# Kernel optimization log

Hardware: AMD Instinct MI355X
Metric: run time of the kernel (lower is better)

The kernel has to match this reference:

```python
import jax, jax.numpy as jnp
import numpy as np

NUM_HEADS = 12
HEAD_DIM = 64
HIDDEN = NUM_HEADS * HEAD_DIM  # 768
B, L = 4, 512

def setup_inputs() -> dict:
    key = jax.random.key(0)
    ks = jax.random.split(key, 8)
    s = 0.02
    return {
        "hidden_states": jax.random.normal(ks[0], (B, L, HIDDEN), jnp.float32),
        "relation_embedding_k": jax.random.normal(ks[1], (B, L, L, HEAD_DIM), jnp.float32),
        "relation_embedding_v": jax.random.normal(ks[2], (B, L, L, HEAD_DIM), jnp.float32),
        "Wq": jax.random.normal(ks[3], (HIDDEN, HIDDEN), jnp.float32) * s,
        "bq": jnp.zeros((HIDDEN,), jnp.float32),
        "Wk": jax.random.normal(ks[4], (HIDDEN, HIDDEN), jnp.float32) * s,
        "bk": jnp.zeros((HIDDEN,), jnp.float32),
        "Wv": jax.random.normal(ks[5], (HIDDEN, HIDDEN), jnp.float32) * s,
        "bv": jnp.zeros((HIDDEN,), jnp.float32),
    }

def _heads(x):
    # [B, L, HIDDEN] -> [B, H, L, D]
    b, l, _ = x.shape
    return x.reshape(b, l, NUM_HEADS, HEAD_DIM).transpose(0, 2, 1, 3)

def reference(hidden_states, relation_embedding_k, relation_embedding_v,
              Wq, bq, Wk, bk, Wv, bv):
    q = _heads(hidden_states @ Wq + bq)  # [B,H,L,D]
    k = _heads(hidden_states @ Wk + bk)
    v = _heads(hidden_states @ Wv + bv)

    # content scores + relation key scores (shared across heads)
    scores = jnp.einsum('bhld,bhmd->bhlm', q, k)
    scores = scores + jnp.einsum('bhld,blrd->bhlr', q, relation_embedding_k)
    scores = scores / np.sqrt(HEAD_DIM).astype(np.float32)

    probs = jax.nn.softmax(scores, axis=-1)  # [B,H,L,L]

    ctx = jnp.einsum('bhlm,bhmd->bhld', probs, v)
    ctx = ctx + jnp.einsum('bhlr,brld->bhld', probs, relation_embedding_v)

    # [B,H,L,D] -> [B,L,HIDDEN]
    b, h, l, d = ctx.shape
    return ctx.transpose(0, 2, 1, 3).reshape(b, l, h * d)
```

## Files before the change

### kernel.cpp

```cpp
#include <hip/hip_runtime.h>
#include <stdint.h>


typedef __attribute__((ext_vector_type(8))) short bf16x8;
typedef __attribute__((ext_vector_type(4))) float f32x4;
typedef __attribute__((ext_vector_type(4))) unsigned int u32x4;

__device__ __forceinline__ unsigned short f2bf(float f) {
  union { float f; unsigned int u; } v; v.f = f;
  unsigned int r = v.u + 0x7fffu + ((v.u >> 16) & 1u);
  return (unsigned short)(r >> 16);
}
__device__ __forceinline__ float bf2f(unsigned short s) {
  union { unsigned int u; float f; } v; v.u = ((unsigned int)s) << 16;
  return v.f;
}
__device__ __forceinline__ void gload_lds16(const void* g, void* l) {
  __builtin_amdgcn_global_load_lds((const __attribute__((address_space(1))) void*)g,
                                   (__attribute__((address_space(3))) void*)l, 16, 0, 0);
}

__global__ void k_cvt_hidden(const float* __restrict__ x, unsigned short* __restrict__ y) {
  int i = blockIdx.x * 256 + threadIdx.x;
  float4 v = reinterpret_cast<const float4*>(x)[i];
  ushort4 o;
  o.x = f2bf(v.x); o.y = f2bf(v.y); o.z = f2bf(v.z); o.w = f2bf(v.w);
  reinterpret_cast<ushort4*>(y)[i] = o;
}

__global__ void k_transp_w(const float* __restrict__ Wq, const float* __restrict__ Wk,
                           const float* __restrict__ Wv, unsigned short* __restrict__ wt) {
  __shared__ float t[64][65];
  const int kt = blockIdx.x, nt = blockIdx.y, wsel = blockIdx.z;
  const float* W = wsel == 0 ? Wq : (wsel == 1 ? Wk : Wv);
  const int lx = threadIdx.x & 63, ly = threadIdx.x >> 6;
  for (int i = 0; i < 64; i += 4)
    t[ly + i][lx] = W[(size_t)(kt * 64 + ly + i) * 768 + nt * 64 + lx];
  __syncthreads();
  for (int i = 0; i < 64; i += 4) {
    int r = ly + i;
    wt[((size_t)wsel * 768 + nt * 64 + r) * 768 + kt * 64 + lx] = f2bf(t[lx][r]);
  }
}

__global__ __launch_bounds__(256) void k_qkv_gemm(
    const unsigned short* __restrict__ A,
    const unsigned short* __restrict__ Bt,
    const float* __restrict__ bq, const float* __restrict__ bk, const float* __restrict__ bv,
    unsigned short* __restrict__ qbf,
    unsigned short* __restrict__ kbf,
    unsigned short* __restrict__ vbt) {
  __shared__ __align__(16) unsigned short lA[64 * 64];
  __shared__ __align__(16) unsigned short lB[64 * 64];
  const int tid = threadIdx.x, lane = tid & 63, w = tid >> 6;
  const int m0 = blockIdx.x * 64, n0 = blockIdx.y * 64;
  const int wm = (w >> 1) * 32, wn = (w & 1) * 32;
  f32x4 acc[2][2] = {};

  for (int kt = 0; kt < 12; ++kt) {
    __syncthreads();
#pragma unroll
    for (int i = 0; i < 2; ++i) {
      int e16 = i * 256 + tid;
      int row = e16 >> 3;
      int kb = (e16 & 7) * 16;
      int dst = row * 128 + (kb ^ ((row & 7) << 4));
      u32x4 va = *(const u32x4*)((const char*)A + (size_t)(m0 + row) * 1536 + kt * 128 + kb);
      *(u32x4*)((char*)lA + dst) = va;
      u32x4 vb = *(const u32x4*)((const char*)Bt + (size_t)(n0 + row) * 1536 + kt * 128 + kb);
      *(u32x4*)((char*)lB + dst) = vb;
    }
    __syncthreads();
#pragma unroll
    for (int ks = 0; ks < 2; ++ks) {
      bf16x8 fa[2], fb[2];
      const int kbyte = (ks * 32 + (lane >> 4) * 8) * 2;
#pragma unroll
      for (int mi = 0; mi < 2; ++mi) {
        int row = wm + mi * 16 + (lane & 15);
        fa[mi] = *(const bf16x8*)((const char*)lA + row * 128 + (kbyte ^ ((row & 7) << 4)));
      }
#pragma unroll
      for (int ni = 0; ni < 2; ++ni) {
        int row = wn + ni * 16 + (lane & 15);
        fb[ni] = *(const bf16x8*)((const char*)lB + row * 128 + (kbyte ^ ((row & 7) << 4)));
      }
#pragma unroll
      for (int mi = 0; mi < 2; ++mi)
#pragma unroll
        for (int ni = 0; ni < 2; ++ni)
          acc[mi][ni] = __builtin_amdgcn_mfma_f32_16x16x32_bf16(fa[mi], fb[ni], acc[mi][ni], 0, 0, 0);
    }
  }
#pragma unroll
  for (int mi = 0; mi < 2; ++mi)
#pragma unroll
    for (int ni = 0; ni < 2; ++ni) {
      int gn = n0 + wn + ni * 16 + (lane & 15);
      float bias = (gn < 768) ? bq[gn] : (gn < 1536 ? bk[gn - 768] : bv[gn - 1536]);
#pragma unroll
      for (int r = 0; r < 4; ++r) {
        int gm = m0 + wm + mi * 16 + ((lane >> 4) << 2) + r;
        float val = acc[mi][ni][r] + bias;
        int b = gm >> 9, l = gm & 511;
        int d = gn & 63;
        if (gn < 768) {
          int h = gn >> 6;
          qbf[(((size_t)(b * 12 + h)) * 512 + l) * 64 + d] = f2bf(val);
        } else if (gn < 1536) {
          int h = (gn - 768) >> 6;
          kbf[(((size_t)(b * 12 + h)) * 512 + l) * 64 + d] = f2bf(val);
        } else {
          int h = (gn - 1536) >> 6;
          vbt[(((size_t)(b * 12 + h)) * 64 + d) * 512 + l] = f2bf(val);
        }
      }
    }
}

__global__ __launch_bounds__(256) void k_scores(
    const unsigned short* __restrict__ qbf, const unsigned short* __restrict__ kbf,
    float* __restrict__ S) {
  __shared__ __align__(16) unsigned short lQ[64 * 64];
  __shared__ __align__(16) unsigned short lK[64 * 64];
  const int tid = threadIdx.x, lane = tid & 63, w = tid >> 6;
  const int mt = blockIdx.x, lt = blockIdx.y, bh = blockIdx.z;
  const int wm = (w >> 1) * 32, wn = (w & 1) * 32;
  f32x4 acc[2][2] = {};
#pragma unroll
  for (int i = 0; i < 2; ++i) {
    int e16 = i * 256 + tid;
    int row = e16 >> 3;
    int kb = (e16 & 7) * 16;
    int dst = row * 128 + (kb ^ ((row & 7) << 4));
    u32x4 vq = *(const u32x4*)((const char*)qbf + ((size_t)bh * 512 + lt * 64 + row) * 128 + kb);
    *(u32x4*)((char*)lQ + dst) = vq;
    u32x4 vk = *(const u32x4*)((const char*)kbf + ((size_t)bh * 512 + mt * 64 + row) * 128 + kb);
    *(u32x4*)((char*)lK + dst) = vk;
  }
  __syncthreads();
#pragma unroll
  for (int ks = 0; ks < 2; ++ks) {
    bf16x8 fa[2], fb[2];
    const int kbyte = (ks * 32 + (lane >> 4) * 8) * 2;
#pragma unroll
    for (int mi = 0; mi < 2; ++mi) {
      int row = wm + mi * 16 + (lane & 15);
      fa[mi] = *(const bf16x8*)((const char*)lQ + row * 128 + (kbyte ^ ((row & 7) << 4)));
    }
#pragma unroll
    for (int ni = 0; ni < 2; ++ni) {
      int row = wn + ni * 16 + (lane & 15);
      fb[ni] = *(const bf16x8*)((const char*)lK + row * 128 + (kbyte ^ ((row & 7) << 4)));
    }
#pragma unroll
    for (int mi = 0; mi < 2; ++mi)
#pragma unroll
      for (int ni = 0; ni < 2; ++ni)
        acc[mi][ni] = __builtin_amdgcn_mfma_f32_16x16x32_bf16(fa[mi], fb[ni], acc[mi][ni], 0, 0, 0);
  }
#pragma unroll
  for (int mi = 0; mi < 2; ++mi)
#pragma unroll
    for (int ni = 0; ni < 2; ++ni) {
      int gm = mt * 64 + wn + ni * 16 + (lane & 15);
#pragma unroll
      for (int r = 0; r < 4; ++r) {
        int gl = lt * 64 + wm + mi * 16 + ((lane >> 4) << 2) + r;
        S[(size_t)bh * 262144 + (size_t)gl * 512 + gm] = acc[mi][ni][r];
      }
    }
}

__global__ __launch_bounds__(256) void k_rel1(
    const unsigned short* __restrict__ qbf,
    const float* __restrict__ relk,
    const float* __restrict__ S,
    unsigned short* __restrict__ pbf) {
  __shared__ __align__(16) float qs[12 * 64];
  __shared__ __align__(16) float rk[64 * 64];
  const int tid = threadIdx.x, lane = tid & 63, w = tid >> 6;
  const int bl = blockIdx.x;
  const int b = bl >> 9, l = bl & 511;

  for (int i = tid; i < 768; i += 256) {
    int h = i >> 6, d = i & 63;
    qs[i] = bf2f(qbf[(((size_t)(b * 12 + h)) * 512 + l) * 64 + d]);
  }

  float acc[3][8];
#pragma unroll
  for (int hh = 0; hh < 3; ++hh)
#pragma unroll
    for (int j = 0; j < 8; ++j) acc[hh][j] = 0.f;

  const char* relk_base = (const char*)relk + (size_t)bl * 131072;
#pragma unroll
  for (int t8 = 0; t8 < 8; ++t8) {
    __syncthreads();
    {
      const char* gbase = relk_base + t8 * 16384;
#pragma unroll
      for (int i = 0; i < 4; ++i) {
        int slot = i * 256 + tid;
        int row = slot >> 4, x = slot & 15;
        const void* src = gbase + row * 256 + ((x * 16) ^ ((row & 7) << 4));
        gload_lds16(src, (char*)rk + (size_t)(i * 256 + w * 64) * 16);
      }
    }
    __syncthreads();
#pragma unroll 4
    for (int dc = 0; dc < 16; ++dc) {
      f32x4 rv = *(const f32x4*)((const char*)rk + lane * 256 + ((dc * 16) ^ ((lane & 7) << 4)));
#pragma unroll
      for (int hh = 0; hh < 3; ++hh) {
        f32x4 q4 = *(const f32x4*)&qs[(w * 3 + hh) * 64 + dc * 4];
        acc[hh][t8] += rv.x * q4.x + rv.y * q4.y + rv.z * q4.z + rv.w * q4.w;
      }
    }
  }

#pragma unroll
  for (int hh = 0; hh < 3; ++hh) {
    int h = w * 3 + hh;
    size_t srow = (((size_t)(b * 12 + h)) * 512 + l) * 512;
    float mx = -1e30f;
#pragma unroll
    for (int j = 0; j < 8; ++j) {
      float s = (acc[hh][j] + S[srow + j * 64 + lane]) * 0.125f;
      acc[hh][j] = s;
      mx = fmaxf(mx, s);
    }
#pragma unroll
    for (int off = 32; off; off >>= 1) mx = fmaxf(mx, __shfl_xor(mx, off));
    float sm = 0.f;
#pragma unroll
    for (int j = 0; j < 8; ++j) { acc[hh][j] = __expf(acc[hh][j] - mx); sm += acc[hh][j]; }
#pragma unroll
    for (int off = 32; off; off >>= 1) sm += __shfl_xor(sm, off);
    float inv = 1.f / sm;
#pragma unroll
    for (int j = 0; j < 8; ++j)
      pbf[srow + j * 64 + lane] = f2bf(acc[hh][j] * inv);
  }
}

__global__ __launch_bounds__(256) void k_rel2(
    const unsigned short* __restrict__ pbf,
    const float* __restrict__ relv,
    float* __restrict__ crel) {
  __shared__ __align__(16) float red[4][12][64];
  const int tid = threadIdx.x, lane = tid & 63, w = tid >> 6;
  const int bl = blockIdx.x;
  const int b = bl >> 9, l = bl & 511;

  float acc[12];
#pragma unroll
  for (int h = 0; h < 12; ++h) acc[h] = 0.f;

  const float* vbase = relv + ((size_t)b * 512 * 512 + (size_t)l) * 64 + lane;
  const unsigned short* pb0 = pbf + ((size_t)b * 12 * 512 + l) * 512;

#pragma unroll 2
  for (int rc = 0; rc < 32; ++rc) {
    int r0 = w * 128 + rc * 4;
    float v0 = vbase[(size_t)(r0 + 0) * 32768];
    float v1 = vbase[(size_t)(r0 + 1) * 32768];
    float v2 = vbase[(size_t)(r0 + 2) * 32768];
    float v3 = vbase[(size_t)(r0 + 3) * 32768];
#pragma unroll
    for (int h = 0; h < 12; ++h) {
      ushort4 p4 = *(const ushort4*)(pb0 + (size_t)h * 262144 + r0);
      acc[h] += bf2f(p4.x) * v0 + bf2f(p4.y) * v1 + bf2f(p4.z) * v2 + bf2f(p4.w) * v3;
    }
  }

#pragma unroll
  for (int h = 0; h < 12; ++h) red[w][h][lane] = acc[h];
  __syncthreads();
  for (int i = tid; i < 768; i += 256) {
    int h = i >> 6, d = i & 63;
    crel[(size_t)bl * 768 + i] =
        red[0][h][d] + red[1][h][d] + red[2][h][d] + red[3][h][d];
  }
}

__global__ __launch_bounds__(256) void k_pv(
    const unsigned short* __restrict__ pbf,
    const unsigned short* __restrict__ vbt,
    const float* __restrict__ crel,
    float* __restrict__ out) {
  __shared__ __align__(16) unsigned short lP[64 * 64];
  __shared__ __align__(16) unsigned short lV[64 * 64];
  const int tid = threadIdx.x, lane = tid & 63, w = tid >> 6;
  const int lt = blockIdx.x, bh = blockIdx.y;
  const int b = bh / 12, h = bh % 12;
  const int wm = (w >> 1) * 32, wn = (w & 1) * 32;
  f32x4 acc[2][2] = {};
  const char* pbase = (const char*)pbf + ((size_t)bh * 512 + lt * 64) * 1024;
  const char* vbase = (const char*)vbt + (size_t)bh * 64 * 1024;
  for (int kt = 0; kt < 8; ++kt) {
    __syncthreads();
#pragma unroll
    for (int i = 0; i < 2; ++i) {
      int e16 = i * 256 + tid;
      int row = e16 >> 3;
      int kb = (e16 & 7) * 16;
      int dst = row * 128 + (kb ^ ((row & 7) << 4));
      u32x4 vp = *(const u32x4*)(pbase + (size_t)row * 1024 + kt * 128 + kb);
      *(u32x4*)((char*)lP + dst) = vp;
      u32x4 vv = *(const u32x4*)(vbase + (size_t)row * 1024 + kt * 128 + kb);
      *(u32x4*)((char*)lV + dst) = vv;
    }
    __syncthreads();
#pragma unroll
    for (int ks = 0; ks < 2; ++ks) {
      bf16x8 fa[2], fb[2];
      const int kbyte = (ks * 32 + (lane >> 4) * 8) * 2;
#pragma unroll
      for (int mi = 0; mi < 2; ++mi) {
        int row = wm + mi * 16 + (lane & 15);
        fa[mi] = *(const bf16x8*)((const char*)lP + row * 128 + (kbyte ^ ((row & 7) << 4)));
      }
#pragma unroll
      for (int ni = 0; ni < 2; ++ni) {
        int row = wn + ni * 16 + (lane & 15);
        fb[ni] = *(const bf16x8*)((const char*)lV + row * 128 + (kbyte ^ ((row & 7) << 4)));
      }
#pragma unroll
      for (int mi = 0; mi < 2; ++mi)
#pragma unroll
        for (int ni = 0; ni < 2; ++ni)
          acc[mi][ni] = __builtin_amdgcn_mfma_f32_16x16x32_bf16(fa[mi], fb[ni], acc[mi][ni], 0, 0, 0);
    }
  }
#pragma unroll
  for (int mi = 0; mi < 2; ++mi)
#pragma unroll
    for (int ni = 0; ni < 2; ++ni) {
      int gd = wn + ni * 16 + (lane & 15);
#pragma unroll
      for (int r = 0; r < 4; ++r) {
        int gl = lt * 64 + wm + mi * 16 + ((lane >> 4) << 2) + r;
        size_t o = ((size_t)b * 512 + gl) * 768 + h * 64 + gd;
        out[o] = acc[mi][ni][r] + crel[o];
      }
    }
}

extern "C" void kernel_launch(void* const* d_in, const int* in_sizes, int n_in,
                              void* d_out, int out_size, void* d_ws, size_t ws_size,
                              hipStream_t stream) {
  (void)in_sizes; (void)n_in; (void)out_size; (void)ws_size;
  const float* hidden = (const float*)d_in[0];
  const float* relk   = (const float*)d_in[1];
  const float* relv   = (const float*)d_in[2];
  const float* Wq     = (const float*)d_in[3];
  const float* bq     = (const float*)d_in[4];
  const float* Wk     = (const float*)d_in[5];
  const float* bk     = (const float*)d_in[6];
  const float* Wv     = (const float*)d_in[7];
  const float* bv     = (const float*)d_in[8];
  float* out = (float*)d_out;
  char* ws = (char*)d_ws;

  unsigned short* hb  = (unsigned short*)(ws);
  unsigned short* wt  = (unsigned short*)(ws + 3145728);
  unsigned short* qbf = (unsigned short*)(ws + 6684672);
  unsigned short* kbf = (unsigned short*)(ws + 9830400);
  unsigned short* vbt = (unsigned short*)(ws + 12976128);
  float*          S   = (float*)(ws + 16121856);
  unsigned short* pbf = (unsigned short*)(ws + 66453504);
  float*          cr  = (float*)(ws + 91619328);

  k_cvt_hidden<<<1536, 256, 0, stream>>>(hidden, hb);
  k_transp_w<<<dim3(12, 12, 3), 256, 0, stream>>>(Wq, Wk, Wv, wt);
  k_qkv_gemm<<<dim3(32, 36), 256, 0, stream>>>(hb, wt, bq, bk, bv, qbf, kbf, vbt);
  k_scores<<<dim3(8, 8, 48), 256, 0, stream>>>(qbf, kbf, S);
  k_rel1<<<2048, 256, 0, stream>>>(qbf, relk, S, pbf);
  k_rel2<<<2048, 256, 0, stream>>>(pbf, relv, cr);
  k_pv<<<dim3(8, 48), 256, 0, stream>>>(pbf, vbt, cr, out);
}
```

Before: 225.6 us.

## Fuse relation-key softmax and relation-value kernels with double-buffered relk staging

Merges k_rel1 and k_rel2 into one kernel, k_rel. Each block keeps its bf16 probability rows in LDS and uses them directly for the relation-value accumulation, instead of re-reading them from global memory in a second launch. The relation-key tile loads are also double-buffered, so the next 16KB tile is fetched while the current one is computed, with one barrier per iteration. This removes a kernel launch and the global round-trip of the probabilities. In exchange, LDS per block grows to about 47KB, which may reduce occupancy.

```diff
diff --git a/kernel.cpp b/kernel.cpp
--- a/kernel.cpp
+++ b/kernel.cpp
@@ -172,13 +172,16 @@
     }
 }
 
-__global__ __launch_bounds__(256) void k_rel1(
+__global__ __launch_bounds__(256) void k_rel(
     const unsigned short* __restrict__ qbf,
     const float* __restrict__ relk,
+    const float* __restrict__ relv,
     const float* __restrict__ S,
-    unsigned short* __restrict__ pbf) {
-  __shared__ __align__(16) float qs[12 * 64];
-  __shared__ __align__(16) float rk[64 * 64];
+    unsigned short* __restrict__ pbf,
+    float* __restrict__ crel) {
+  __shared__ __align__(16) float qs[768];
+  __shared__ __align__(16) unsigned short ps[12 * 512];
+  __shared__ __align__(16) char rk[2][16384];
   const int tid = threadIdx.x, lane = tid & 63, w = tid >> 6;
   const int bl = blockIdx.x;
   const int b = bl >> 9, l = bl & 511;
@@ -188,37 +191,42 @@
     qs[i] = bf2f(qbf[(((size_t)(b * 12 + h)) * 512 + l) * 64 + d]);
   }
 
+  const char* relk_base = (const char*)relk + (size_t)bl * 131072;
+#define STAGE(t, buf)                                                        \
+  {                                                                          \
+    const char* gbase = relk_base + (t) * 16384;                             \
+    _Pragma("unroll")                                                        \
+    for (int i = 0; i < 4; ++i) {                                            \
+      int slot = i * 256 + tid;                                              \
+      int row = slot >> 4, x = slot & 15;                                    \
+      const void* src = gbase + row * 256 + ((x * 16) ^ ((row & 7) << 4));   \
+      gload_lds16(src, &rk[buf][(size_t)(i * 256 + w * 64) * 16]);           \
+    }                                                                        \
+  }
+
   float acc[3][8];
 #pragma unroll
   for (int hh = 0; hh < 3; ++hh)
 #pragma unroll
     for (int j = 0; j < 8; ++j) acc[hh][j] = 0.f;
 
-  const char* relk_base = (const char*)relk + (size_t)bl * 131072;
-#pragma unroll
-  for (int t8 = 0; t8 < 8; ++t8) {
-    __syncthreads();
-    {
-      const char* gbase = relk_base + t8 * 16384;
-#pragma unroll
-      for (int i = 0; i < 4; ++i) {
-        int slot = i * 256 + tid;
-        int row = slot >> 4, x = slot & 15;
-        const void* src = gbase + row * 256 + ((x * 16) ^ ((row & 7) << 4));
-        gload_lds16(src, (char*)rk + (size_t)(i * 256 + w * 64) * 16);
-      }
-    }
-    __syncthreads();
+  STAGE(0, 0);
+  __syncthreads();
+#pragma unroll
+  for (int t = 0; t < 8; ++t) {
+    if (t < 7) STAGE(t + 1, (t + 1) & 1);
 #pragma unroll 4
     for (int dc = 0; dc < 16; ++dc) {
-      f32x4 rv = *(const f32x4*)((const char*)rk + lane * 256 + ((dc * 16) ^ ((lane & 7) << 4)));
+      f32x4 rv = *(const f32x4*)(&rk[t & 1][0] + lane * 256 + ((dc * 16) ^ ((lane & 7) << 4)));
 #pragma unroll
       for (int hh = 0; hh < 3; ++hh) {
         f32x4 q4 = *(const f32x4*)&qs[(w * 3 + hh) * 64 + dc * 4];
-        acc[hh][t8] += rv.x * q4.x + rv.y * q4.y + rv.z * q4.z + rv.w * q4.w;
-      }
-    }
-  }
+        acc[hh][t] += rv.x * q4.x + rv.y * q4.y + rv.z * q4.z + rv.w * q4.w;
+      }
+    }
+    __syncthreads();
+  }
+#undef STAGE
 
 #pragma unroll
   for (int hh = 0; hh < 3; ++hh) {
@@ -240,27 +248,18 @@
     for (int off = 32; off; off >>= 1) sm += __shfl_xor(sm, off);
     float inv = 1.f / sm;
 #pragma unroll
-    for (int j = 0; j < 8; ++j)
-      pbf[srow + j * 64 + lane] = f2bf(acc[hh][j] * inv);
-  }
-}
-
-__global__ __launch_bounds__(256) void k_rel2(
-    const unsigned short* __restrict__ pbf,
-    const float* __restrict__ relv,
-    float* __restrict__ crel) {
-  __shared__ __align__(16) float red[4][12][64];
-  const int tid = threadIdx.x, lane = tid & 63, w = tid >> 6;
-  const int bl = blockIdx.x;
-  const int b = bl >> 9, l = bl & 511;
-
-  float acc[12];
-#pragma unroll
-  for (int h = 0; h < 12; ++h) acc[h] = 0.f;
-
+    for (int j = 0; j < 8; ++j) {
+      unsigned short pb = f2bf(acc[hh][j] * inv);
+      ps[h * 512 + j * 64 + lane] = pb;
+      pbf[srow + j * 64 + lane] = pb;
+    }
+  }
+  __syncthreads();
+
+  float cacc[12];
+#pragma unroll
+  for (int h = 0; h < 12; ++h) cacc[h] = 0.f;
   const float* vbase = relv + ((size_t)b * 512 * 512 + (size_t)l) * 64 + lane;
-  const unsigned short* pb0 = pbf + ((size_t)b * 12 * 512 + l) * 512;
-
 #pragma unroll 2
   for (int rc = 0; rc < 32; ++rc) {
     int r0 = w * 128 + rc * 4;
@@ -270,18 +269,18 @@
     float v3 = vbase[(size_t)(r0 + 3) * 32768];
 #pragma unroll
     for (int h = 0; h < 12; ++h) {
-      ushort4 p4 = *(const ushort4*)(pb0 + (size_t)h * 262144 + r0);
-      acc[h] += bf2f(p4.x) * v0 + bf2f(p4.y) * v1 + bf2f(p4.z) * v2 + bf2f(p4.w) * v3;
-    }
-  }
-
-#pragma unroll
-  for (int h = 0; h < 12; ++h) red[w][h][lane] = acc[h];
+      ushort4 p4 = *(const ushort4*)&ps[h * 512 + r0];
+      cacc[h] += bf2f(p4.x) * v0 + bf2f(p4.y) * v1 + bf2f(p4.z) * v2 + bf2f(p4.w) * v3;
+    }
+  }
+  float* red = (float*)rk;
+#pragma unroll
+  for (int h = 0; h < 12; ++h) red[(w * 12 + h) * 64 + lane] = cacc[h];
   __syncthreads();
   for (int i = tid; i < 768; i += 256) {
     int h = i >> 6, d = i & 63;
     crel[(size_t)bl * 768 + i] =
-        red[0][h][d] + red[1][h][d] + red[2][h][d] + red[3][h][d];
+        red[h * 64 + d] + red[(12 + h) * 64 + d] + red[(24 + h) * 64 + d] + red[(36 + h) * 64 + d];
   }
 }
 
@@ -377,7 +376,6 @@
   k_transp_w<<<dim3(12, 12, 3), 256, 0, stream>>>(Wq, Wk, Wv, wt);
   k_qkv_gemm<<<dim3(32, 36), 256, 0, stream>>>(hb, wt, bq, bk, bv, qbf, kbf, vbt);
   k_scores<<<dim3(8, 8, 48), 256, 0, stream>>>(qbf, kbf, S);
-  k_rel1<<<2048, 256, 0, stream>>>(qbf, relk, S, pbf);
-  k_rel2<<<2048, 256, 0, stream>>>(pbf, relv, cr);
+  k_rel<<<2048, 256, 0, stream>>>(qbf, relk, relv, S, pbf, cr);
   k_pv<<<dim3(8, 48), 256, 0, stream>>>(pbf, vbt, cr, out);
 }
```

Result: faster. 200.1 us (-11.3%).
